# Performance work log

Hardware: AMD Instinct MI355X
Metric: run time of the kernel (lower is better)

## Reference

```python
import jax, jax.numpy as jnp
import numpy as np
import math

V, T, E, H, L = 32000, 1024, 1024, 16, 6
B = 2
D = E // H
F = 4 * E


def setup_inputs() -> dict:
    key = jax.random.key(0)
    ks = jax.random.split(key, 12)
    s = 0.02
    rn = lambda k, shape: jax.random.normal(k, shape, jnp.float32) * s
    return dict(
        idx=jax.random.randint(ks[0], (B, T), 0, V),
        tok_w=rn(ks[1], (V, E)),
        pos_w=rn(ks[2], (T, E)),
        ln1_g=jnp.ones((L, E)), ln1_b=jnp.zeros((L, E)),
        wq=rn(ks[3], (L, E, E)), wk=rn(ks[4], (L, E, E)), wv=rn(ks[5], (L, E, E)),
        wp=rn(ks[6], (L, E, E)), bp=jnp.zeros((L, E)),
        ln2_g=jnp.ones((L, E)), ln2_b=jnp.zeros((L, E)),
        w1=rn(ks[7], (L, E, F)), b1=jnp.zeros((L, F)),
        w2=rn(ks[8], (L, F, E)), b2=jnp.zeros((L, E)),
        lnf_g=jnp.ones((E,)), lnf_b=jnp.zeros((E,)),
        wlm=rn(ks[9], (E, V)), blm=jnp.zeros((V,)),
    )


def _layernorm(x, g, b, eps=1e-5):
    m = jnp.mean(x, axis=-1, keepdims=True)
    v = jnp.var(x, axis=-1, keepdims=True)
    return (x - m) * jax.lax.rsqrt(v + eps) * g + b


def _forward(idx, tok_w, pos_w, ln1_g, ln1_b, wq, wk, wv, wp, bp,
             ln2_g, ln2_b, w1, b1, w2, b2, lnf_g, lnf_b, wlm, blm):
    Bx, Tx = idx.shape
    x = tok_w[idx] + pos_w[jnp.arange(Tx)][None, :, :]  # [B,T,E]
    causal = jnp.tril(jnp.ones((Tx, Tx), dtype=bool))
    scale = 1.0 / math.sqrt(D)
    for l in range(L):
        h = _layernorm(x, ln1_g[l], ln1_b[l])
        q = (h @ wq[l]).reshape(Bx, Tx, H, D).transpose(0, 2, 1, 3)  # [B,H,T,D]
        k = (h @ wk[l]).reshape(Bx, Tx, H, D).transpose(0, 2, 1, 3)
        v = (h @ wv[l]).reshape(Bx, Tx, H, D).transpose(0, 2, 1, 3)
        att = jnp.einsum('bhtd,bhsd->bhts', q, k) * scale  # [B,H,T,T]
        att = jnp.where(causal, att, -jnp.inf)
        att = jax.nn.softmax(att, axis=-1)
        y = jnp.einsum('bhts,bhsd->bhtd', att, v)
        y = y.transpose(0, 2, 1, 3).reshape(Bx, Tx, E)
        x = x + y @ wp[l] + bp[l]
        h2 = _layernorm(x, ln2_g[l], ln2_b[l])
        ff = jax.nn.gelu(h2 @ w1[l] + b1[l], approximate=False) @ w2[l] + b2[l]
        x = x + ff
    x = _layernorm(x, lnf_g, lnf_b)
    return x @ wlm + blm  # logits [B,T,V]


def reference(idx, tok_w, pos_w, ln1_g, ln1_b, wq, wk, wv, wp, bp,
              ln2_g, ln2_b, w1, b1, w2, b2, lnf_g, lnf_b, wlm, blm):
    return _forward(idx, tok_w, pos_w, ln1_g, ln1_b, wq, wk, wv, wp, bp,
                    ln2_g, ln2_b, w1, b1, w2, b2, lnf_g, lnf_b, wlm, blm)
```

## Files before the change

kernel.cpp:

```cpp
#include <hip/hip_runtime.h>

#define T_SEQ   1024
#define E_DIM   1024
#define H_HEADS 16
#define D_HEAD  64
#define L_LAYERS 6
#define B_BATCH 2
#define F_DIM   4096
#define V_VOCAB 32000

typedef float f32x4 __attribute__((ext_vector_type(4)));
typedef short short8 __attribute__((ext_vector_type(8)));

__device__ __forceinline__ unsigned short f2bf(float f) {
  union { float f; unsigned int u; } v; v.f = f;
  unsigned int r = v.u + 0x7fffu + ((v.u >> 16) & 1u);
  return (unsigned short)(r >> 16);
}

#define GLDS16(gp, lp) __builtin_amdgcn_global_load_lds( \
    (const __attribute__((address_space(1))) void*)(gp), \
    (__attribute__((address_space(3))) void*)(lp), 16, 0, 0)

__global__ void embed_kernel(const int* __restrict__ idx, const float* __restrict__ tok,
                             const float* __restrict__ pos, float* __restrict__ x) {
  int i = blockIdx.x * 256 + threadIdx.x;
  int bt = i >> 8;
  int e4 = i & 255;
  int t  = bt & (T_SEQ - 1);
  int tokid = idx[bt];
  f32x4 a = *(const f32x4*)(tok + (size_t)tokid * E_DIM + e4 * 4);
  f32x4 p = *(const f32x4*)(pos + (size_t)t * E_DIM + e4 * 4);
  *(f32x4*)(x + (size_t)bt * E_DIM + e4 * 4) = a + p;
}

__global__ void ln_kernel(const float* __restrict__ x, const float* __restrict__ g,
                          const float* __restrict__ b, unsigned short* __restrict__ out) {
  int row = blockIdx.x;
  int tid = threadIdx.x;
  const float* xr = x + (size_t)row * E_DIM;
  f32x4 v = *(const f32x4*)(xr + tid * 4);
  float s  = v[0] + v[1] + v[2] + v[3];
  float s2 = v[0]*v[0] + v[1]*v[1] + v[2]*v[2] + v[3]*v[3];
  #pragma unroll
  for (int off = 32; off > 0; off >>= 1) {
    s  += __shfl_xor(s,  off);
    s2 += __shfl_xor(s2, off);
  }
  __shared__ float red[2][4];
  int wave = tid >> 6;
  if ((tid & 63) == 0) { red[0][wave] = s; red[1][wave] = s2; }
  __syncthreads();
  s  = red[0][0] + red[0][1] + red[0][2] + red[0][3];
  s2 = red[1][0] + red[1][1] + red[1][2] + red[1][3];
  float mean = s * (1.0f / E_DIM);
  float var  = s2 * (1.0f / E_DIM) - mean * mean;
  float rstd = rsqrtf(var + 1e-5f);
  f32x4 gv = *(const f32x4*)(g + tid * 4);
  f32x4 bv = *(const f32x4*)(b + tid * 4);
  ushort4 o;
  o.x = f2bf((v[0] - mean) * rstd * gv[0] + bv[0]);
  o.y = f2bf((v[1] - mean) * rstd * gv[1] + bv[1]);
  o.z = f2bf((v[2] - mean) * rstd * gv[2] + bv[2]);
  o.w = f2bf((v[3] - mean) * rstd * gv[3] + bv[3]);
  *(ushort4*)(out + (size_t)row * E_DIM + tid * 4) = o;
}

__device__ __forceinline__ void wtrans_body(const float* __restrict__ W,
    unsigned short* __restrict__ Wt, int K, int N, int bx, int by) {
  __shared__ float tile[64][65];
  const int n0 = bx * 64, k0 = by * 64;
  const int tr  = threadIdx.x >> 4;
  const int tc4 = (threadIdx.x & 15) * 4;
  #pragma unroll
  for (int p = 0; p < 4; ++p) {
    f32x4 v = *(const f32x4*)(W + (size_t)(k0 + p * 16 + tr) * N + n0 + tc4);
    tile[p * 16 + tr][tc4 + 0] = v[0];
    tile[p * 16 + tr][tc4 + 1] = v[1];
    tile[p * 16 + tr][tc4 + 2] = v[2];
    tile[p * 16 + tr][tc4 + 3] = v[3];
  }
  __syncthreads();
  #pragma unroll
  for (int p = 0; p < 4; ++p) {
    int n = p * 16 + tr;
    ushort4 o;
    o.x = f2bf(tile[tc4 + 0][n]);
    o.y = f2bf(tile[tc4 + 1][n]);
    o.z = f2bf(tile[tc4 + 2][n]);
    o.w = f2bf(tile[tc4 + 3][n]);
    *(ushort4*)(Wt + (size_t)(n0 + n) * K + k0 + tc4) = o;
  }
}

__global__ __launch_bounds__(256) void wtrans_kernel(const float* __restrict__ W,
    unsigned short* __restrict__ Wt, int K, int N) {
  wtrans_body(W, Wt, K, N, blockIdx.x, blockIdx.y);
}

__global__ __launch_bounds__(256) void wtrans4_kernel(const float* __restrict__ W0,
    const float* __restrict__ W1, const float* __restrict__ W2, const float* __restrict__ W3,
    unsigned short* __restrict__ Wt) {
  const float* W = blockIdx.z == 0 ? W0 : (blockIdx.z == 1 ? W1 : (blockIdx.z == 2 ? W2 : W3));
  wtrans_body(W, Wt + (size_t)blockIdx.z * E_DIM * E_DIM, E_DIM, E_DIM,
              blockIdx.x, blockIdx.y);
}

__global__ __launch_bounds__(256) void wtrans2_kernel(const float* __restrict__ W1,
    const float* __restrict__ W2, unsigned short* __restrict__ Wt1,
    unsigned short* __restrict__ Wt2) {
  const int id = blockIdx.x;
  if (blockIdx.y == 0) wtrans_body(W1, Wt1, E_DIM, F_DIM, id % (F_DIM / 64), id / (F_DIM / 64));
  else                 wtrans_body(W2, Wt2, F_DIM, E_DIM, id % (E_DIM / 64), id / (E_DIM / 64));
}

__global__ __launch_bounds__(512) void attn_mfma_kernel(
    const unsigned short* __restrict__ qk, const unsigned short* __restrict__ vt,
    unsigned short* __restrict__ y) {
  __shared__ __align__(16) unsigned short Kl[64 * 64];
  __shared__ __align__(16) unsigned short Vl[64 * 64];
  __shared__ __align__(16) unsigned short pbuf[8][16][72];
  const int tid  = threadIdx.x;
  const int lane = tid & 63;
  const int wave = tid >> 6;
  const int grp  = wave >> 2;
  const int wl   = wave & 3;
  const int bx = blockIdx.x;
  const int h  = blockIdx.y & (H_HEADS - 1);
  const int b  = blockIdx.y >> 4;
  const int qt = grp == 0 ? (15 - bx) : bx;
  const int r0 = qt * 64 + wl * 16;
  const size_t RS = 2 * E_DIM;
  const unsigned short* q = qk + (size_t)b * T_SEQ * RS + (size_t)h * D_HEAD;
  const unsigned short* k = q + E_DIM;
  const unsigned short* vb = vt + (size_t)(b * H_HEADS + h) * D_HEAD * T_SEQ;
  const size_t ybase = (size_t)b * T_SEQ * E_DIM + (size_t)h * D_HEAD;
  const int fr = lane & 15, fg = lane >> 4;
  const int rsw = (fr & 7) << 4;
  const int srow = lane >> 3;
  const int ssw  = ((lane & 7) * 16) ^ (srow << 4);

  short8 aq[2];
  #pragma unroll
  for (int c = 0; c < 2; ++c)
    aq[c] = *(const short8*)(q + (size_t)(r0 + fr) * RS + c * 32 + fg * 8);

  f32x4 oacc[4];
  #pragma unroll
  for (int cg = 0; cg < 4; ++cg) oacc[cg] = (f32x4){0.f, 0.f, 0.f, 0.f};
  float m_ = -1e30f, l_ = 0.0f;

  char* pb = (char*)pbuf + wave * 16 * 144;
  const int ntiles = 16 - bx;
  for (int t = 0; t < ntiles; ++t) {
    const int j0 = t * 64;
    __syncthreads();
    GLDS16((const char*)k + (size_t)(j0 + wave * 8 + srow) * RS * 2 + ssw,
           (char*)Kl + wave * 8 * 128);
    GLDS16((const char*)vb + ((size_t)(wave * 8 + srow) * T_SEQ + j0) * 2 + ssw,
           (char*)Vl + wave * 8 * 128);
    __syncthreads();
    if (t <= qt) {
      f32x4 st[4];
      #pragma unroll
      for (int c = 0; c < 4; ++c) {
        const char* kb = (char*)Kl + (c * 16 + fr) * 128;
        short8 ka0 = *(const short8*)(kb + ((fg * 16) ^ rsw));
        short8 ka1 = *(const short8*)(kb + ((64 + fg * 16) ^ rsw));
        f32x4 z = (f32x4){0.f, 0.f, 0.f, 0.f};
        z = __builtin_amdgcn_mfma_f32_16x16x32_bf16(ka0, aq[0], z, 0, 0, 0);
        z = __builtin_amdgcn_mfma_f32_16x16x32_bf16(ka1, aq[1], z, 0, 0, 0);
        st[c] = z;
      }
      const int qg = r0 + fr;
      float pv[4][4];
      float mx = -1e30f;
      #pragma unroll
      for (int c = 0; c < 4; ++c)
        #pragma unroll
        for (int r = 0; r < 4; ++r) {
          const int kj = j0 + c * 16 + fg * 4 + r;
          float val = (kj <= qg) ? st[c][r] * 0.125f : -1e30f;
          pv[c][r] = val;
          mx = fmaxf(mx, val);
        }
      mx = fmaxf(mx, __shfl_xor(mx, 16));
      mx = fmaxf(mx, __shfl_xor(mx, 32));
      const float mn = fmaxf(m_, mx);
      const float cfs = __expf(m_ - mn);
      float ls = 0.0f;
      #pragma unroll
      for (int c = 0; c < 4; ++c) {
        ushort4 o;
        float e0 = __expf(pv[c][0] - mn), e1 = __expf(pv[c][1] - mn);
        float e2 = __expf(pv[c][2] - mn), e3 = __expf(pv[c][3] - mn);
        ls += (e0 + e1) + (e2 + e3);
        o.x = f2bf(e0); o.y = f2bf(e1); o.z = f2bf(e2); o.w = f2bf(e3);
        *(ushort4*)(pb + fr * 144 + c * 32 + fg * 8) = o;
      }
      ls += __shfl_xor(ls, 16);
      ls += __shfl_xor(ls, 32);
      l_ = l_ * cfs + ls;
      m_ = mn;
      float cfO[4];
      #pragma unroll
      for (int r = 0; r < 4; ++r) cfO[r] = __shfl(cfs, (lane & 48) | (fg * 4 + r));
      asm volatile("s_waitcnt lgkmcnt(0)" ::: "memory");
      __builtin_amdgcn_sched_barrier(0);
      short8 pa0 = *(const short8*)(pb + fr * 144 + fg * 16);
      short8 pa1 = *(const short8*)(pb + fr * 144 + 64 + fg * 16);
      __builtin_amdgcn_s_setprio(1);
      #pragma unroll
      for (int cg = 0; cg < 4; ++cg) {
        const char* vv = (char*)Vl + (cg * 16 + fr) * 128;
        short8 b0 = *(const short8*)(vv + ((fg * 16) ^ rsw));
        short8 b1 = *(const short8*)(vv + ((64 + fg * 16) ^ rsw));
        #pragma unroll
        for (int r = 0; r < 4; ++r) oacc[cg][r] *= cfO[r];
        oacc[cg] = __builtin_amdgcn_mfma_f32_16x16x32_bf16(pa0, b0, oacc[cg], 0, 0, 0);
        oacc[cg] = __builtin_amdgcn_mfma_f32_16x16x32_bf16(pa1, b1, oacc[cg], 0, 0, 0);
      }
      __builtin_amdgcn_s_setprio(0);
    }
  }
  float lO[4];
  #pragma unroll
  for (int r = 0; r < 4; ++r) lO[r] = __shfl(l_, (lane & 48) | (fg * 4 + r));
  #pragma unroll
  for (int cg = 0; cg < 4; ++cg)
    #pragma unroll
    for (int r = 0; r < 4; ++r)
      y[ybase + (size_t)(r0 + fg * 4 + r) * E_DIM + cg * 16 + fr] = f2bf(oacc[cg][r] / lO[r]);
}

template<int BM, int BN, bool HAS_BIAS, bool GELU_ACT, bool HAS_RES, int OMODE>
__global__ __launch_bounds__(256) void gemm_bt_kernel(
    const unsigned short* __restrict__ A, const unsigned short* __restrict__ Bt,
    const float* __restrict__ bias, const float* __restrict__ res,
    void* __restrict__ out, unsigned short* __restrict__ vt, int M, int N, int K) {
  constexpr int BK = 64;
  constexpr int MR = BM / 32;
  constexpr int NR = BN / 32;
  constexpr int AI = BM / 32;
  constexpr int BI = BN / 32;
  __shared__ __align__(16) unsigned short As[BM * BK];
  __shared__ __align__(16) unsigned short Bs[BN * BK];
  const int tid  = threadIdx.x;
  const int lane = tid & 63;
  const int wave = tid >> 6;
  const int wr = wave >> 1, wc = wave & 1;

  const int mt = M / BM;
  const int q8 = gridDim.x >> 3;
  const int g  = (blockIdx.x & 7) * q8 + (blockIdx.x >> 3);
  const int m0 = (g % mt) * BM, n0 = (g / mt) * BN;

  const int fr = lane & 15, fg = lane >> 4;
  const int lrow = lane >> 3;
  const int scol = ((lane & 7) * 16) ^ (lrow << 4);
  const size_t K2 = (size_t)K * 2;
  const char* aG = (const char*)A  + (size_t)(m0 + wave * 8 + lrow) * K2 + scol;
  const char* bG = (const char*)Bt + (size_t)(n0 + wave * 8 + lrow) * K2 + scol;

  f32x4 acc[MR][NR];
  #pragma unroll
  for (int mi = 0; mi < MR; ++mi)
    #pragma unroll
    for (int ni = 0; ni < NR; ++ni) acc[mi][ni] = (f32x4){0.f, 0.f, 0.f, 0.f};

  for (int k0 = 0; k0 < K; k0 += BK) {
    __syncthreads();
    #pragma unroll
    for (int i = 0; i < AI; ++i)
      GLDS16(aG + (size_t)i * 32 * K2 + (size_t)k0 * 2, (char*)As + wave * 1024 + i * 4096);
    #pragma unroll
    for (int i = 0; i < BI; ++i)
      GLDS16(bG + (size_t)i * 32 * K2 + (size_t)k0 * 2, (char*)Bs + wave * 1024 + i * 4096);
    __syncthreads();

    short8 af[MR][2], bf[NR][2];
    #pragma unroll
    for (int mi = 0; mi < MR; ++mi) {
      const int row = wr * (BM / 2) + mi * 16 + fr;
      #pragma unroll
      for (int kh = 0; kh < 2; ++kh)
        af[mi][kh] = *(const short8*)((const char*)As + row * 128 +
                       ((kh * 64 + fg * 16) ^ ((row & 7) << 4)));
    }
    #pragma unroll
    for (int ni = 0; ni < NR; ++ni) {
      const int row = wc * (BN / 2) + ni * 16 + fr;
      #pragma unroll
      for (int kh = 0; kh < 2; ++kh)
        bf[ni][kh] = *(const short8*)((const char*)Bs + row * 128 +
                       ((kh * 64 + fg * 16) ^ ((row & 7) << 4)));
    }
    #pragma unroll
    for (int mi = 0; mi < MR; ++mi)
      #pragma unroll
      for (int ni = 0; ni < NR; ++ni) {
        acc[mi][ni] = __builtin_amdgcn_mfma_f32_16x16x32_bf16(af[mi][0], bf[ni][0], acc[mi][ni], 0, 0, 0);
        acc[mi][ni] = __builtin_amdgcn_mfma_f32_16x16x32_bf16(af[mi][1], bf[ni][1], acc[mi][ni], 0, 0, 0);
      }
  }

  #pragma unroll
  for (int mi = 0; mi < MR; ++mi) {
    #pragma unroll
    for (int ni = 0; ni < NR; ++ni) {
      const int col = n0 + wc * (BN / 2) + ni * 16 + fr;
      float bv = HAS_BIAS ? bias[col] : 0.0f;
      float vals[4];
      const int rbase = m0 + wr * (BM / 2) + mi * 16 + fg * 4;
      #pragma unroll
      for (int r = 0; r < 4; ++r) {
        float val = acc[mi][ni][r] + bv;
        if (GELU_ACT) val = 0.5f * val * (1.0f + erff(val * 0.70710678118f));
        if (HAS_RES)  val += res[(size_t)(rbase + r) * N + col];
        vals[r] = val;
      }
      if (OMODE == 0) {
        #pragma unroll
        for (int r = 0; r < 4; ++r)
          ((float*)out)[(size_t)(rbase + r) * N + col] = vals[r];
      } else if (OMODE == 1) {
        #pragma unroll
        for (int r = 0; r < 4; ++r)
          ((unsigned short*)out)[(size_t)(rbase + r) * N + col] = f2bf(vals[r]);
      } else {
        if (col < 2 * E_DIM) {
          #pragma unroll
          for (int r = 0; r < 4; ++r)
            ((unsigned short*)out)[(size_t)(rbase + r) * 2 * E_DIM + col] = f2bf(vals[r]);
        } else {
          const int c2 = col - 2 * E_DIM;
          const int hh = c2 >> 6, d = c2 & 63;
          const int bb = rbase >> 10, t0 = rbase & (T_SEQ - 1);
          ushort4 o;
          o.x = f2bf(vals[0]); o.y = f2bf(vals[1]);
          o.z = f2bf(vals[2]); o.w = f2bf(vals[3]);
          *(ushort4*)(vt + ((size_t)(bb * H_HEADS + hh) * D_HEAD + d) * T_SEQ + t0) = o;
        }
      }
    }
  }
}

__global__ __launch_bounds__(512, 1) void gemm8p_kernel(
    const unsigned short* __restrict__ A, const unsigned short* __restrict__ Bt,
    const float* __restrict__ bias, float* __restrict__ out, int M, int N, int K) {
  __shared__ __align__(16) char lds[131072];
  const int tid  = threadIdx.x;
  const int lane = tid & 63;
  const int wv   = tid >> 6;
  const int wm = wv >> 2, wn = wv & 3;

  const int mt = M >> 8;
  const int q8 = gridDim.x >> 3;
  const int g  = (blockIdx.x & 7) * q8 + (blockIdx.x >> 3);
  const int m0 = (g % mt) * 256, n0 = (g / mt) * 256;

  const int fr = lane & 15, fg = lane >> 4;
  const size_t K2 = (size_t)K * 2;
  const int nIter = K >> 7;

  const int csw0 = (fg * 16) ^ ((fr & 7) << 4);
  const int csw1 = (64 + fg * 16) ^ ((fr & 7) << 4);

  const int sc = (lane * 16) & 127;
  const size_t laneoff = (size_t)(lane >> 3) * K2 + (size_t)(sc ^ ((lane >> 3) << 4));
  const char* Asrc = (const char*)(A + (size_t)m0 * K) + (size_t)(wv * 8) * K2 + laneoff;
  const char* Bsrc = (const char*)(Bt + (size_t)n0 * K) + laneoff;

  f32x4 acc[8][4];
  #pragma unroll
  for (int i = 0; i < 8; ++i)
    #pragma unroll
    for (int j = 0; j < 4; ++j) acc[i][j] = (f32x4){0.f, 0.f, 0.f, 0.f};

  auto stageA = [&](int b, int q, int kt) {
    GLDS16(Asrc + (size_t)(q * 64) * K2 + (size_t)kt * 128,
           lds + b * 65536 + q * 8192 + wv * 1024);
  };
  auto stageB = [&](int b, int j, int o, int kt) {
    const int gw = j * 64 + wv * 8;
    const int rw = ((gw >> 5) << 6) + (gw & 31) + o * 32;
    GLDS16(Bsrc + (size_t)rw * K2 + (size_t)kt * 128,
           lds + b * 65536 + 32768 + rw * 128);
  };

  stageA(0, 0, 0); stageA(0, 2, 0);
  stageB(0, 0, 0, 0); stageB(0, 1, 0, 0);
  stageA(0, 1, 0); stageA(0, 3, 0);
  stageB(0, 0, 1, 0); stageB(0, 1, 1, 0);
  stageA(1, 0, 1); stageA(1, 2, 1);
  stageB(1, 0, 0, 1); stageB(1, 1, 0, 1);
  __builtin_amdgcn_sched_barrier(0);
  asm volatile("s_waitcnt vmcnt(4)" ::: "memory");
  __builtin_amdgcn_s_barrier();

  for (int i = 0; i < nIter; ++i) {
    const bool last = (i == nIter - 1);
    #pragma unroll
    for (int p = 0; p < 8; ++p) {
      const int b  = p >> 2;
      const int mh = (p & 3) >> 1;
      const int nh = p & 1;
      const char* Ab = lds + b * 65536;
      const char* Bb = Ab + 32768;
      __builtin_amdgcn_sched_barrier(0);
      short8 fa[4][2], fb[2][2];
      #pragma unroll
      for (int j = 0; j < 4; ++j) {
        const int row = wm * 128 + mh * 64 + j * 16 + fr;
        fa[j][0] = *(const short8*)(Ab + row * 128 + csw0);
        fa[j][1] = *(const short8*)(Ab + row * 128 + csw1);
      }
      #pragma unroll
      for (int n = 0; n < 2; ++n) {
        const int row = wn * 64 + nh * 32 + n * 16 + fr;
        fb[n][0] = *(const short8*)(Bb + row * 128 + csw0);
        fb[n][1] = *(const short8*)(Bb + row * 128 + csw1);
      }
      if (p == 0) { stageA(1, 1, 2 * i + 1); stageA(1, 3, 2 * i + 1); }
      if (p == 1) { stageB(1, 0, 1, 2 * i + 1); stageB(1, 1, 1, 2 * i + 1); }
      if (!last) {
        if (p == 2) { stageA(0, 0, 2 * i + 2); stageA(0, 2, 2 * i + 2); }
        if (p == 3) { stageB(0, 0, 0, 2 * i + 2); stageB(0, 1, 0, 2 * i + 2); }
        if (p == 4) { stageA(0, 1, 2 * i + 2); stageA(0, 3, 2 * i + 2); }
        if (p == 5) { stageB(0, 0, 1, 2 * i + 2); stageB(0, 1, 1, 2 * i + 2); }
        if (p == 6) { stageA(1, 0, 2 * i + 3); stageA(1, 2, 2 * i + 3); }
        if (p == 7) { stageB(1, 0, 0, 2 * i + 3); stageB(1, 1, 0, 2 * i + 3); }
      }
      __builtin_amdgcn_sched_barrier(0);
      __builtin_amdgcn_s_barrier();
      __builtin_amdgcn_sched_barrier(0);
      __builtin_amdgcn_s_setprio(1);
      #pragma unroll
      for (int j = 0; j < 4; ++j)
        #pragma unroll
        for (int n = 0; n < 2; ++n) {
          acc[mh * 4 + j][nh * 2 + n] = __builtin_amdgcn_mfma_f32_16x16x32_bf16(
              fa[j][0], fb[n][0], acc[mh * 4 + j][nh * 2 + n], 0, 0, 0);
          acc[mh * 4 + j][nh * 2 + n] = __builtin_amdgcn_mfma_f32_16x16x32_bf16(
              fa[j][1], fb[n][1], acc[mh * 4 + j][nh * 2 + n], 0, 0, 0);
        }
      __builtin_amdgcn_s_setprio(0);
      __builtin_amdgcn_sched_barrier(0);
      if (p == 3) {
        if (!last) asm volatile("s_waitcnt vmcnt(4)" ::: "memory");
        else       asm volatile("s_waitcnt vmcnt(0)" ::: "memory");
      }
      if (p == 7 && !last)
        asm volatile("s_waitcnt vmcnt(4)" ::: "memory");
      __builtin_amdgcn_s_barrier();
    }
  }

  #pragma unroll
  for (int mi = 0; mi < 8; ++mi) {
    #pragma unroll
    for (int ni = 0; ni < 4; ++ni) {
      const int col = n0 + wn * 64 + ni * 16 + fr;
      const float bv = bias[col];
      #pragma unroll
      for (int r = 0; r < 4; ++r) {
        const int row = m0 + wm * 128 + mi * 16 + fg * 4 + r;
        out[(size_t)row * N + col] = acc[mi][ni][r] + bv;
      }
    }
  }
}

extern "C" void kernel_launch(void* const* d_in, const int* in_sizes, int n_in,
                              void* d_out, int out_size, void* d_ws, size_t ws_size,
                              hipStream_t stream) {
  const int*   idx   = (const int*)  d_in[0];
  const float* tok_w = (const float*)d_in[1];
  const float* pos_w = (const float*)d_in[2];
  const float* ln1_g = (const float*)d_in[3];
  const float* ln1_b = (const float*)d_in[4];
  const float* wq    = (const float*)d_in[5];
  const float* wk    = (const float*)d_in[6];
  const float* wv    = (const float*)d_in[7];
  const float* wp    = (const float*)d_in[8];
  const float* bp    = (const float*)d_in[9];
  const float* ln2_g = (const float*)d_in[10];
  const float* ln2_b = (const float*)d_in[11];
  const float* w1    = (const float*)d_in[12];
  const float* b1    = (const float*)d_in[13];
  const float* w2    = (const float*)d_in[14];
  const float* b2    = (const float*)d_in[15];
  const float* lnf_g = (const float*)d_in[16];
  const float* lnf_b = (const float*)d_in[17];
  const float* wlm   = (const float*)d_in[18];
  const float* blm   = (const float*)d_in[19];

  const int M = B_BATCH * T_SEQ;
  const size_t EE = (size_t)E_DIM * E_DIM;
  const size_t EF = (size_t)E_DIM * F_DIM;
  char* p = (char*)d_ws;
  float* x            = (float*)p;          p += (size_t)M * E_DIM * 4;
  unsigned short* hb  = (unsigned short*)p; p += (size_t)M * E_DIM * 2;
  unsigned short* qkb = (unsigned short*)p; p += (size_t)M * 2 * E_DIM * 2;
  unsigned short* vtb = (unsigned short*)p; p += (size_t)M * E_DIM * 2;
  unsigned short* yb  = (unsigned short*)p; p += (size_t)M * E_DIM * 2;
  unsigned short* tb  = (unsigned short*)p; p += (size_t)M * F_DIM * 2;
  unsigned short* wtb = (unsigned short*)p; p += (size_t)V_VOCAB * E_DIM * 2;

  embed_kernel<<<M * E_DIM / 4 / 256, 256, 0, stream>>>(idx, tok_w, pos_w, x);

  for (int l = 0; l < L_LAYERS; ++l) {
    ln_kernel<<<M, 256, 0, stream>>>(x, ln1_g + (size_t)l * E_DIM, ln1_b + (size_t)l * E_DIM, hb);
    wtrans4_kernel<<<dim3(E_DIM / 64, E_DIM / 64, 4), 256, 0, stream>>>(
        wq + l * EE, wk + l * EE, wv + l * EE, wp + l * EE, wtb);
    gemm_bt_kernel<128, 128, false, false, false, 2>
        <<<(M / 128) * (3 * E_DIM / 128), 256, 0, stream>>>(
        hb, wtb, nullptr, nullptr, qkb, vtb, M, 3 * E_DIM, E_DIM);
    attn_mfma_kernel<<<dim3(8, B_BATCH * H_HEADS), 512, 0, stream>>>(qkb, vtb, yb);
    gemm_bt_kernel<64, 128, true, false, true, 0>
        <<<(M / 64) * (E_DIM / 128), 256, 0, stream>>>(
        yb, wtb + 3 * EE, bp + (size_t)l * E_DIM, x, x, nullptr, M, E_DIM, E_DIM);
    ln_kernel<<<M, 256, 0, stream>>>(x, ln2_g + (size_t)l * E_DIM, ln2_b + (size_t)l * E_DIM, hb);
    wtrans2_kernel<<<dim3(1024, 2), 256, 0, stream>>>(
        w1 + l * EF, w2 + l * EF, wtb, wtb + EF);
    gemm_bt_kernel<128, 128, true, true, false, 1>
        <<<(M / 128) * (F_DIM / 128), 256, 0, stream>>>(
        hb, wtb, b1 + (size_t)l * F_DIM, nullptr, tb, nullptr, M, F_DIM, E_DIM);
    gemm_bt_kernel<64, 128, true, false, true, 0>
        <<<(M / 64) * (E_DIM / 128), 256, 0, stream>>>(
        tb, wtb + EF, b2 + (size_t)l * E_DIM, x, x, nullptr, M, E_DIM, F_DIM);
  }
  ln_kernel<<<M, 256, 0, stream>>>(x, lnf_g, lnf_b, hb);
  wtrans_kernel<<<dim3(V_VOCAB / 64, E_DIM / 64), 256, 0, stream>>>(wlm, wtb, E_DIM, V_VOCAB);
  gemm8p_kernel<<<(M / 256) * (V_VOCAB / 256), 512, 0, stream>>>(
      hb, wtb, blm, (float*)d_out, M, V_VOCAB, E_DIM);
}
```

Measured before the change: 1.357 ms.

## Split attention KV tiles across wave groups with double-buffered loads and merge

Each attention block now handles a single query tile, and its two 4-wave groups each process half of every 64-key tile; the two partial softmax states are merged through shared memory at the end. K/V tiles are double-buffered so the load of the next tile overlaps compute on the current one. The grid doubles to 16x32 blocks, with causal load balancing based on batch index. This aims to raise parallelism and hide global-load latency in exchange for more shared memory and an extra merge step per block.

Measured after the change: 1.325 ms. 2.3% less time.

```diff
diff --git a/kernel.cpp b/kernel.cpp
--- a/kernel.cpp
+++ b/kernel.cpp
@@ -117,28 +117,27 @@
 __global__ __launch_bounds__(512) void attn_mfma_kernel(
     const unsigned short* __restrict__ qk, const unsigned short* __restrict__ vt,
     unsigned short* __restrict__ y) {
-  __shared__ __align__(16) unsigned short Kl[64 * 64];
-  __shared__ __align__(16) unsigned short Vl[64 * 64];
-  __shared__ __align__(16) unsigned short pbuf[8][16][72];
+  __shared__ __align__(16) char smem[2 * 16384 + 8 * 1280 + 512];
   const int tid  = threadIdx.x;
   const int lane = tid & 63;
   const int wave = tid >> 6;
-  const int grp  = wave >> 2;
-  const int wl   = wave & 3;
-  const int bx = blockIdx.x;
+  const int wl = wave & 3;
+  const int g  = wave >> 2;
+  const int qx = blockIdx.x;
   const int h  = blockIdx.y & (H_HEADS - 1);
   const int b  = blockIdx.y >> 4;
-  const int qt = grp == 0 ? (15 - bx) : bx;
+  const int qt = b ? (15 - qx) : qx;
   const int r0 = qt * 64 + wl * 16;
   const size_t RS = 2 * E_DIM;
-  const unsigned short* q = qk + (size_t)b * T_SEQ * RS + (size_t)h * D_HEAD;
-  const unsigned short* k = q + E_DIM;
+  const unsigned short* q  = qk + (size_t)b * T_SEQ * RS + (size_t)h * D_HEAD;
+  const unsigned short* k  = q + E_DIM;
   const unsigned short* vb = vt + (size_t)(b * H_HEADS + h) * D_HEAD * T_SEQ;
   const size_t ybase = (size_t)b * T_SEQ * E_DIM + (size_t)h * D_HEAD;
   const int fr = lane & 15, fg = lane >> 4;
-  const int rsw = (fr & 7) << 4;
   const int srow = lane >> 3;
   const int ssw  = ((lane & 7) * 16) ^ (srow << 4);
+  char* pb = smem + 32768 + wave * 1280;
+  float* mlb = (float*)(smem + 32768 + 10240);
 
   short8 aq[2];
   #pragma unroll
@@ -150,38 +149,53 @@
   for (int cg = 0; cg < 4; ++cg) oacc[cg] = (f32x4){0.f, 0.f, 0.f, 0.f};
   float m_ = -1e30f, l_ = 0.0f;
 
-  char* pb = (char*)pbuf + wave * 16 * 144;
-  const int ntiles = 16 - bx;
-  for (int t = 0; t < ntiles; ++t) {
+  auto stage = [&](int t) {
     const int j0 = t * 64;
-    __syncthreads();
-    GLDS16((const char*)k + (size_t)(j0 + wave * 8 + srow) * RS * 2 + ssw,
-           (char*)Kl + wave * 8 * 128);
+    char* Kd = smem + (t & 1) * 16384;
+    GLDS16((const char*)k  + (size_t)(j0 + wave * 8 + srow) * RS * 2 + ssw,
+           Kd + wave * 1024);
     GLDS16((const char*)vb + ((size_t)(wave * 8 + srow) * T_SEQ + j0) * 2 + ssw,
-           (char*)Vl + wave * 8 * 128);
-    __syncthreads();
-    if (t <= qt) {
-      f32x4 st[4];
-      #pragma unroll
-      for (int c = 0; c < 4; ++c) {
-        const char* kb = (char*)Kl + (c * 16 + fr) * 128;
-        short8 ka0 = *(const short8*)(kb + ((fg * 16) ^ rsw));
-        short8 ka1 = *(const short8*)(kb + ((64 + fg * 16) ^ rsw));
+           Kd + 8192 + wave * 1024);
+  };
+
+  stage(0);
+  for (int t = 0; t <= qt; ++t) {
+    __builtin_amdgcn_sched_barrier(0);
+    __builtin_amdgcn_s_barrier();
+    if (t < qt) stage(t + 1);
+    __builtin_amdgcn_sched_barrier(0);
+    if (t < qt) asm volatile("s_waitcnt vmcnt(2)" ::: "memory");
+    else        asm volatile("s_waitcnt vmcnt(0)" ::: "memory");
+    __builtin_amdgcn_sched_barrier(0);
+    __builtin_amdgcn_s_barrier();
+    __builtin_amdgcn_sched_barrier(0);
+    const char* Kl = smem + (t & 1) * 16384;
+    const char* Vl = Kl + 8192;
+    const int j0 = t * 64;
+    if (!(t == qt && g == 1 && wl < 2)) {
+      f32x4 st[2];
+      #pragma unroll
+      for (int cc = 0; cc < 2; ++cc) {
+        const int kloc = g * 32 + cc * 16 + fr;
+        const char* kb = Kl + kloc * 128;
+        const int sw = (kloc & 7) << 4;
+        short8 ka0 = *(const short8*)(kb + ((fg * 16) ^ sw));
+        short8 ka1 = *(const short8*)(kb + ((64 + fg * 16) ^ sw));
         f32x4 z = (f32x4){0.f, 0.f, 0.f, 0.f};
         z = __builtin_amdgcn_mfma_f32_16x16x32_bf16(ka0, aq[0], z, 0, 0, 0);
         z = __builtin_amdgcn_mfma_f32_16x16x32_bf16(ka1, aq[1], z, 0, 0, 0);
-        st[c] = z;
+        st[cc] = z;
       }
       const int qg = r0 + fr;
-      float pv[4][4];
+      float pv[2][4];
       float mx = -1e30f;
       #pragma unroll
-      for (int c = 0; c < 4; ++c)
+      for (int cc = 0; cc < 2; ++cc)
         #pragma unroll
         for (int r = 0; r < 4; ++r) {
-          const int kj = j0 + c * 16 + fg * 4 + r;
-          float val = (kj <= qg) ? st[c][r] * 0.125f : -1e30f;
-          pv[c][r] = val;
+          const int kj = j0 + g * 32 + cc * 16 + fg * 4 + r;
+          float val = (kj <= qg) ? st[cc][r] * 0.125f : -1e30f;
+          pv[cc][r] = val;
           mx = fmaxf(mx, val);
         }
       mx = fmaxf(mx, __shfl_xor(mx, 16));
@@ -190,13 +204,15 @@
       const float cfs = __expf(m_ - mn);
       float ls = 0.0f;
       #pragma unroll
-      for (int c = 0; c < 4; ++c) {
+      for (int cc = 0; cc < 2; ++cc) {
         ushort4 o;
-        float e0 = __expf(pv[c][0] - mn), e1 = __expf(pv[c][1] - mn);
-        float e2 = __expf(pv[c][2] - mn), e3 = __expf(pv[c][3] - mn);
+        float e0 = pv[cc][0] > -1e29f ? __expf(pv[cc][0] - mn) : 0.0f;
+        float e1 = pv[cc][1] > -1e29f ? __expf(pv[cc][1] - mn) : 0.0f;
+        float e2 = pv[cc][2] > -1e29f ? __expf(pv[cc][2] - mn) : 0.0f;
+        float e3 = pv[cc][3] > -1e29f ? __expf(pv[cc][3] - mn) : 0.0f;
         ls += (e0 + e1) + (e2 + e3);
         o.x = f2bf(e0); o.y = f2bf(e1); o.z = f2bf(e2); o.w = f2bf(e3);
-        *(ushort4*)(pb + fr * 144 + c * 32 + fg * 8) = o;
+        *(ushort4*)(pb + fr * 80 + cc * 32 + fg * 8) = o;
       }
       ls += __shfl_xor(ls, 16);
       ls += __shfl_xor(ls, 32);
@@ -207,30 +223,51 @@
       for (int r = 0; r < 4; ++r) cfO[r] = __shfl(cfs, (lane & 48) | (fg * 4 + r));
       asm volatile("s_waitcnt lgkmcnt(0)" ::: "memory");
       __builtin_amdgcn_sched_barrier(0);
-      short8 pa0 = *(const short8*)(pb + fr * 144 + fg * 16);
-      short8 pa1 = *(const short8*)(pb + fr * 144 + 64 + fg * 16);
+      short8 pa = *(const short8*)(pb + fr * 80 + fg * 16);
       __builtin_amdgcn_s_setprio(1);
       #pragma unroll
       for (int cg = 0; cg < 4; ++cg) {
-        const char* vv = (char*)Vl + (cg * 16 + fr) * 128;
-        short8 b0 = *(const short8*)(vv + ((fg * 16) ^ rsw));
-        short8 b1 = *(const short8*)(vv + ((64 + fg * 16) ^ rsw));
+        const int d = cg * 16 + fr;
+        short8 bv = *(const short8*)(Vl + d * 128 + ((g * 64 + fg * 16) ^ ((d & 7) << 4)));
         #pragma unroll
         for (int r = 0; r < 4; ++r) oacc[cg][r] *= cfO[r];
-        oacc[cg] = __builtin_amdgcn_mfma_f32_16x16x32_bf16(pa0, b0, oacc[cg], 0, 0, 0);
-        oacc[cg] = __builtin_amdgcn_mfma_f32_16x16x32_bf16(pa1, b1, oacc[cg], 0, 0, 0);
+        oacc[cg] = __builtin_amdgcn_mfma_f32_16x16x32_bf16(pa, bv, oacc[cg], 0, 0, 0);
       }
       __builtin_amdgcn_s_setprio(0);
     }
   }
-  float lO[4];
-  #pragma unroll
-  for (int r = 0; r < 4; ++r) lO[r] = __shfl(l_, (lane & 48) | (fg * 4 + r));
-  #pragma unroll
-  for (int cg = 0; cg < 4; ++cg)
-    #pragma unroll
-    for (int r = 0; r < 4; ++r)
-      y[ybase + (size_t)(r0 + fg * 4 + r) * E_DIM + cg * 16 + fr] = f2bf(oacc[cg][r] / lO[r]);
+  __syncthreads();
+  float* obuf = (float*)smem;
+  if (g == 1) {
+    #pragma unroll
+    for (int cg = 0; cg < 4; ++cg)
+      #pragma unroll
+      for (int r = 0; r < 4; ++r)
+        obuf[wl * 1024 + (fg * 4 + r) * 64 + cg * 16 + fr] = oacc[cg][r];
+    if (fg == 0) { mlb[(wl * 16 + fr) * 2] = m_; mlb[(wl * 16 + fr) * 2 + 1] = l_; }
+  }
+  __syncthreads();
+  if (g == 0) {
+    const float m1 = mlb[(wl * 16 + fr) * 2];
+    const float l1 = mlb[(wl * 16 + fr) * 2 + 1];
+    const float m  = fmaxf(m_, m1);
+    const float c0 = __expf(m_ - m), c1 = __expf(m1 - m);
+    const float li = 1.0f / (l_ * c0 + l1 * c1);
+    float c0O[4], c1O[4], liO[4];
+    #pragma unroll
+    for (int r = 0; r < 4; ++r) {
+      const int src = (lane & 48) | (fg * 4 + r);
+      c0O[r] = __shfl(c0, src); c1O[r] = __shfl(c1, src); liO[r] = __shfl(li, src);
+    }
+    #pragma unroll
+    for (int cg = 0; cg < 4; ++cg)
+      #pragma unroll
+      for (int r = 0; r < 4; ++r) {
+        const float o1 = obuf[wl * 1024 + (fg * 4 + r) * 64 + cg * 16 + fr];
+        const float val = (oacc[cg][r] * c0O[r] + o1 * c1O[r]) * liO[r];
+        y[ybase + (size_t)(r0 + fg * 4 + r) * E_DIM + cg * 16 + fr] = f2bf(val);
+      }
+  }
 }
 
 template<int BM, int BN, bool HAS_BIAS, bool GELU_ACT, bool HAS_RES, int OMODE>
@@ -517,7 +554,7 @@
     gemm_bt_kernel<128, 128, false, false, false, 2>
         <<<(M / 128) * (3 * E_DIM / 128), 256, 0, stream>>>(
         hb, wtb, nullptr, nullptr, qkb, vtb, M, 3 * E_DIM, E_DIM);
-    attn_mfma_kernel<<<dim3(8, B_BATCH * H_HEADS), 512, 0, stream>>>(qkb, vtb, yb);
+    attn_mfma_kernel<<<dim3(16, B_BATCH * H_HEADS), 512, 0, stream>>>(qkb, vtb, yb);
     gemm_bt_kernel<64, 128, true, false, true, 0>
         <<<(M / 64) * (E_DIM / 128), 256, 0, stream>>>(
         yb, wtb + 3 * EE, bp + (size_t)l * E_DIM, x, x, nullptr, M, E_DIM, E_DIM);
```
